# Kernel optimization log

Measured on AMD Instinct MI355X. Metric: run time of the kernel, lower is better.

The kernel has to match this reference:

```python
import jax, jax.numpy as jnp
import numpy as np

B_, N, C = 1024, 64, 512
H = 16          # num_heads
NW = 64         # number of windows (B_ % NW == 0)


def setup_inputs() -> dict:
    key = jax.random.key(0)
    ks = jax.random.split(key, 7)
    return {
        "x": jax.random.normal(ks[0], (B_, N, C), jnp.float32),
        "mask": jax.random.normal(ks[1], (NW, N, N), jnp.float32),
        "qkv_w": jax.random.normal(ks[2], (C, 3 * C), jnp.float32) * 0.02,
        "qkv_b": jax.random.normal(ks[3], (3 * C,), jnp.float32) * 0.02,
        "proj_w": jax.random.normal(ks[4], (C, C), jnp.float32) * 0.02,
        "proj_b": jax.random.normal(ks[5], (C,), jnp.float32) * 0.02,
        "bias_table": jax.random.normal(ks[6], (2 * N - 1, H), jnp.float32) * 0.02,
    }


def reference(x, mask, qkv_w, qkv_b, proj_w, proj_b, bias_table):
    b_, n, c = x.shape
    h = bias_table.shape[1]
    ws = (bias_table.shape[0] + 1) // 2  # window_size, == n here
    d = c // h
    scale = d ** -0.5

    qkv = x @ qkv_w + qkv_b                                   # [B_, N, 3C]
    qkv = qkv.reshape(b_, n, 3, h, d).transpose(2, 0, 3, 1, 4)  # [3, B_, H, N, d]
    q, k, v = qkv[0] * scale, qkv[1], qkv[2]

    attn = jnp.einsum('bhnd,bhmd->bhnm', q, k)                # [B_, H, N, N]

    coords = jnp.arange(ws)
    rel_idx = coords[:, None] - coords[None, :] + ws - 1       # [ws, ws]
    bias = bias_table[rel_idx].transpose(2, 0, 1)              # [H, ws, ws]
    attn = attn + bias[None]

    nw = mask.shape[0]
    attn = attn.reshape(b_ // nw, nw, h, n, n) + mask[None, :, None]
    attn = attn.reshape(-1, h, n, n)
    attn = jax.nn.softmax(attn, axis=-1)

    out = jnp.einsum('bhnm,bhmd->bhnd', attn, v)               # [B_, H, N, d]
    # Faithful to the TF code: v keeps a leading singleton dim after tf.split,
    # so attn@v is [1, B_, H, N, d]; perm [0,2,1,3,4] swaps B_ and H before
    # the final reshape to (B_, N, C).
    out = out[None].transpose(0, 2, 1, 3, 4).reshape(b_, n, c)
    return out @ proj_w + proj_b
```

## Files before the change

kernel.cpp:

```cpp
#include <hip/hip_runtime.h>
#include <hip/hip_bf16.h>
#include <stdint.h>

typedef __attribute__((ext_vector_type(4))) float f32x4;
typedef __attribute__((ext_vector_type(8))) short s16x8;

__device__ __forceinline__ short f2bf(float f) {
  union { float f; uint32_t u; } v; v.f = f;
  uint32_t r = v.u + 0x7FFFu + ((v.u >> 16) & 1u);
  return (short)(r >> 16);
}
__device__ __forceinline__ uint32_t pack2bf(float a, float b) {
  return (uint32_t)(uint16_t)f2bf(a) | ((uint32_t)(uint16_t)f2bf(b) << 16);
}

__device__ __forceinline__ void async16(const void* g, void* l) {
  __builtin_amdgcn_global_load_lds(
      (const __attribute__((address_space(1))) void*)g,
      (__attribute__((address_space(3))) void*)l, 16, 0, 0);
}

__device__ __forceinline__ void transpose_tile(const float* __restrict__ in,
                                               short* __restrict__ out,
                                               int K, int N, int bx, int by, int t) {
  __shared__ float tile[64][65];
  const int tx = t & 63, ty = t >> 6;
#pragma unroll
  for (int r = ty; r < 64; r += 4)
    tile[r][tx] = in[(size_t)(by * 64 + r) * N + bx * 64 + tx];
  __syncthreads();
#pragma unroll
  for (int r = ty; r < 64; r += 4)
    out[(size_t)(bx * 64 + r) * K + by * 64 + tx] = f2bf(tile[tx][r]);
}

__global__ __launch_bounds__(256) void k_prep(const float* __restrict__ x,
                                              short* __restrict__ xbf,
                                              const float* __restrict__ qkv_w,
                                              short* __restrict__ wT,
                                              const float* __restrict__ proj_w,
                                              short* __restrict__ projT) {
  const int bid = blockIdx.x, t = threadIdx.x;
  if (bid < 16384) {
    int i = bid * 256 + t;
    const float4* p = (const float4*)x + (size_t)i * 2;
    float4 a = p[0], b = p[1];
    s16x8 o;
    o[0] = f2bf(a.x); o[1] = f2bf(a.y); o[2] = f2bf(a.z); o[3] = f2bf(a.w);
    o[4] = f2bf(b.x); o[5] = f2bf(b.y); o[6] = f2bf(b.z); o[7] = f2bf(b.w);
    ((s16x8*)xbf)[i] = o;
  } else if (bid < 16384 + 192) {
    int idx = bid - 16384;
    transpose_tile(qkv_w, wT, 512, 1536, idx % 24, idx / 24, t);
  } else {
    int idx = bid - 16384 - 192;
    transpose_tile(proj_w, projT, 512, 512, idx % 8, idx / 8, t);
  }
}

#define TILE_SH 16384

template <int OUTMODE, int NBN, int KK>
__global__ __launch_bounds__(512, 2) void k_gemm256p(const short* __restrict__ A,
                                                     const short* __restrict__ Bw,
                                                     const float* __restrict__ bias,
                                                     void* __restrict__ C,
                                                     int N, int nrounds) {
  __shared__ short lds[2 * 2 * TILE_SH];
  const int t = threadIdx.x;
  const int w = t >> 6, l = t & 63;
  const int wm = w >> 2, wn = w & 3;
  const int swz = (((int)blockIdx.x & 7) << 5) + ((int)blockIdx.x >> 3);

  const int NT = KK >> 6;
  const int NS = nrounds * NT;

  auto stage = [&](const short* __restrict__ G, int row0, int kt, short* dst) {
#pragma unroll
    for (int L = 0; L < 2; ++L) {
      int cw = L * 512 + (t & ~63);
      int c = cw + l;
      int r = c >> 3, s = c & 7;
      async16(G + (size_t)(row0 + r) * KK + kt + ((s ^ (r & 7)) << 3), dst + cw * 8);
    }
  };
  auto issueA = [&](int step, int bmv, int hf) {
    int kt = step & 7;
    stage(A, bmv * 256 + hf * 128, kt * 64, lds + (kt & 1) * 32768 + hf * 8192);
  };
  auto issueB = [&](int step, int bnv, int hf) {
    int kt = step & 7;
    stage(Bw, bnv * 256 + hf * 128, kt * 64, lds + (kt & 1) * 32768 + TILE_SH + hf * 8192);
  };

  const int g = l >> 4, v = l & 7;
  int ofsA[2], ofsB[2];
#pragma unroll
  for (int ks = 0; ks < 2; ++ks) {
    ofsA[ks] = (wm * 128 + (l & 15)) * 64 + (((ks * 4 + g) ^ v) << 3);
    ofsB[ks] = (wn * 64 + (l & 15)) * 64 + (((ks * 4 + g) ^ v) << 3);
  }

  f32x4 acc[8][4] = {};
  s16x8 af[4], bfr[4];

#define RDA4(BASE, KS, AI0)                                           \
  af[0] = *(const s16x8*)((BASE) + ofsA[KS] + ((AI0) + 0) * 1024);    \
  af[1] = *(const s16x8*)((BASE) + ofsA[KS] + ((AI0) + 1) * 1024);    \
  af[2] = *(const s16x8*)((BASE) + ofsA[KS] + ((AI0) + 2) * 1024);    \
  af[3] = *(const s16x8*)((BASE) + ofsA[KS] + ((AI0) + 3) * 1024);

#define RDB4(BASE, KS)                                                \
  bfr[0] = *(const s16x8*)((BASE) + ofsB[KS] + 0 * 1024);             \
  bfr[1] = *(const s16x8*)((BASE) + ofsB[KS] + 1 * 1024);             \
  bfr[2] = *(const s16x8*)((BASE) + ofsB[KS] + 2 * 1024);             \
  bfr[3] = *(const s16x8*)((BASE) + ofsB[KS] + 3 * 1024);

#define MF16(AI0)                                                                                              \
  __builtin_amdgcn_s_setprio(1);                                                                               \
  _Pragma("unroll")                                                                                            \
  for (int nj = 0; nj < 4; ++nj) {                                                                             \
    acc[(AI0) + 0][nj] = __builtin_amdgcn_mfma_f32_16x16x32_bf16(af[0], bfr[nj], acc[(AI0) + 0][nj], 0, 0, 0); \
    acc[(AI0) + 1][nj] = __builtin_amdgcn_mfma_f32_16x16x32_bf16(af[1], bfr[nj], acc[(AI0) + 1][nj], 0, 0, 0); \
    acc[(AI0) + 2][nj] = __builtin_amdgcn_mfma_f32_16x16x32_bf16(af[2], bfr[nj], acc[(AI0) + 2][nj], 0, 0, 0); \
    acc[(AI0) + 3][nj] = __builtin_amdgcn_mfma_f32_16x16x32_bf16(af[3], bfr[nj], acc[(AI0) + 3][nj], 0, 0, 0); \
  }                                                                                                            \
  __builtin_amdgcn_s_setprio(0);

#define PHASE(RD_STMT, STAGE_STMT, AI0, TAIL_STMT)      \
  {                                                     \
    RD_STMT;                                            \
    STAGE_STMT;                                         \
    __builtin_amdgcn_s_barrier();                       \
    asm volatile("s_waitcnt lgkmcnt(0)" ::: "memory");  \
    MF16(AI0);                                          \
    TAIL_STMT;                                          \
    __builtin_amdgcn_s_barrier();                       \
  }

  {
    const int bm0 = swz / NBN, bn0 = swz % NBN;
    issueB(0, bn0, 0); issueB(0, bn0, 1);
    issueA(0, bm0, 0); issueA(0, bm0, 1);
    issueB(1, bn0, 0); issueB(1, bn0, 1);
  }
  asm volatile("s_waitcnt vmcnt(4)" ::: "memory");
  __builtin_amdgcn_s_barrier();

  for (int j = 0; j < nrounds; ++j) {
    const int tauc = swz + (j << 8);
    const int bmc = tauc / NBN, bnc = tauc % NBN;
    for (int T = 0; T < NT; ++T) {
      const int s = (j << 3) + T;
      const int s1 = s + 1, s2 = s + 2;
      const int tau1 = swz + ((s1 >> 3) << 8);
      const int tau2 = swz + ((s2 >> 3) << 8);
      const int bm1 = tau1 / NBN;
      const int bn2 = tau2 % NBN;
      const short* Ab = lds + (T & 1) * 32768;
      const short* Bb = Ab + TILE_SH;

      PHASE(RDB4(Bb, 0); RDA4(Ab, 0, 0), if (s1 < NS) issueA(s1, bm1, 0), 0, );
      PHASE(RDA4(Ab, 0, 4), if (s1 < NS) issueA(s1, bm1, 1), 4, );
      PHASE(RDB4(Bb, 1); RDA4(Ab, 1, 0), if (s2 < NS) issueB(s2, bn2, 0), 0, );
      PHASE(RDA4(Ab, 1, 4), if (s2 < NS) issueB(s2, bn2, 1), 4,
            if (s2 < NS) { asm volatile("s_waitcnt vmcnt(4)" ::: "memory"); }
            else if (s1 < NS) { asm volatile("s_waitcnt vmcnt(0)" ::: "memory"); });
    }

#pragma unroll
    for (int ai = 0; ai < 8; ++ai)
#pragma unroll
      for (int nj = 0; nj < 4; ++nj) {
        int col = bnc * 256 + wn * 64 + nj * 16 + (l & 15);
        float bv = bias[col];
#pragma unroll
        for (int r = 0; r < 4; ++r) {
          int row = bmc * 256 + wm * 128 + ai * 16 + (l >> 4) * 4 + r;
          float vv = acc[ai][nj][r] + bv;
          if (OUTMODE == 1) {
            ((float*)C)[(size_t)row * N + col] = vv;
          } else if (OUTMODE == 0) {
            ((short*)C)[(size_t)row * N + col] = f2bf(vv);
          } else {
            int bb = row >> 6, nn = row & 63;
            int sel = col >> 9, hh = (col >> 5) & 15, dd = col & 31;
            ((short*)C)[(((size_t)(bb * 48 + hh * 3 + sel)) << 11) + (nn << 5) + dd] = f2bf(vv);
          }
        }
      }
#pragma unroll
    for (int ai = 0; ai < 8; ++ai)
#pragma unroll
      for (int nj = 0; nj < 4; ++nj)
        acc[ai][nj] = (f32x4){0.f, 0.f, 0.f, 0.f};
  }
#undef PHASE
#undef MF16
#undef RDA4
#undef RDB4
}

__global__ __launch_bounds__(256) void k_attn(const short* __restrict__ qkv2,
                                              const float* __restrict__ mask,
                                              const float* __restrict__ bias_table,
                                              short* __restrict__ Y) {
  __shared__ __align__(16) float mask_lds[64 * 64];
  __shared__ float bias_lds[4][128];
  __shared__ short p_lds[4][64][72];
  __shared__ short v_lds[4][64][40];

  const int t = threadIdx.x, wv = t >> 6, ln = t & 63;
  const int b = blockIdx.x;
  const int h = blockIdx.y * 4 + wv;
  const int hi = ln >> 4, lo = ln & 15;

  const float4* mk = (const float4*)(mask + (size_t)(b & 63) * 4096);
#pragma unroll
  for (int u = 0; u < 4; ++u) {
    int idx = t + 256 * u;
    int row = idx >> 4, c4 = (idx & 15) * 4;
    *(float4*)&mask_lds[row * 64 + (c4 ^ ((row & 7) << 2))] = mk[idx];
  }
  for (int u = ln; u < 127; u += 64) bias_lds[wv][u] = bias_table[u * 16 + h];

  const short* base = qkv2 + ((size_t)(b * 16 + h)) * 3 * 2048;
  const short* vg = base + 4096;
#pragma unroll
  for (int u = 0; u < 4; ++u) {
    int row = u * 16 + (ln >> 2), c8 = (ln & 3) * 8;
    *(s16x8*)&v_lds[wv][row][c8] = *(const s16x8*)(vg + row * 32 + c8);
  }
  __syncthreads();

  s16x8 qf[4], kf[4];
#pragma unroll
  for (int i = 0; i < 4; ++i) {
    qf[i] = *(const s16x8*)(base + (16 * i + lo) * 32 + hi * 8);
    kf[i] = *(const s16x8*)(base + 2048 + (16 * i + lo) * 32 + hi * 8);
  }
  f32x4 s2[4][4] = {};
#pragma unroll
  for (int j = 0; j < 4; ++j)
#pragma unroll
    for (int i = 0; i < 4; ++i)
      s2[j][i] = __builtin_amdgcn_mfma_f32_16x16x32_bf16(kf[j], qf[i], s2[j][i], 0, 0, 0);

  const float scale = 0.17677669529663687f;
#pragma unroll
  for (int i = 0; i < 4; ++i) {
    const int n = 16 * i + lo;
    const int msw = (n & 7) << 2;
    float x[16];
    float vmax = -1e30f;
#pragma unroll
    for (int j = 0; j < 4; ++j) {
      float4 mrow = *(const float4*)&mask_lds[n * 64 + ((16 * j + 4 * hi) ^ msw)];
#pragma unroll
      for (int r = 0; r < 4; ++r) {
        int m = 16 * j + 4 * hi + r;
        float xx = s2[j][i][r] * scale + bias_lds[wv][n - m + 63] + (&mrow.x)[r];
        x[j * 4 + r] = xx;
        vmax = fmaxf(vmax, xx);
      }
    }
    vmax = fmaxf(vmax, __shfl_xor(vmax, 16, 64));
    vmax = fmaxf(vmax, __shfl_xor(vmax, 32, 64));
    float sum = 0.f;
#pragma unroll
    for (int u = 0; u < 16; ++u) {
      x[u] = __expf(x[u] - vmax);
      sum += x[u];
    }
    sum += __shfl_xor(sum, 16, 64);
    sum += __shfl_xor(sum, 32, 64);
    float rsv = 1.0f / sum;
#pragma unroll
    for (int j = 0; j < 4; ++j)
#pragma unroll
      for (int rp = 0; rp < 2; ++rp)
        *(uint32_t*)&p_lds[wv][n][16 * j + 4 * hi + rp * 2] =
            pack2bf(x[j * 4 + rp * 2] * rsv, x[j * 4 + rp * 2 + 1] * rsv);
  }

  f32x4 o2[2][4] = {};
#pragma unroll
  for (int kk = 0; kk < 2; ++kk) {
    s16x8 pa[4];
#pragma unroll
    for (int i2 = 0; i2 < 4; ++i2)
      pa[i2] = *(const s16x8*)&p_lds[wv][16 * i2 + lo][kk * 32 + hi * 8];
#pragma unroll
    for (int j2 = 0; j2 < 2; ++j2) {
      s16x8 vf;
#pragma unroll
      for (int jj = 0; jj < 8; ++jj)
        vf[jj] = v_lds[wv][kk * 32 + hi * 8 + jj][16 * j2 + lo];
#pragma unroll
      for (int i2 = 0; i2 < 4; ++i2)
        o2[j2][i2] = __builtin_amdgcn_mfma_f32_16x16x32_bf16(vf, pa[i2], o2[j2][i2], 0, 0, 0);
    }
  }

  const int rr = h * 64 + (b >> 4);
#pragma unroll
  for (int i2 = 0; i2 < 4; ++i2) {
    int ss = (b & 15) * 4 + i2;
    short* yr = Y + ((size_t)rr * 64 + ss) * 512 + lo * 32 + 4 * hi;
#pragma unroll
    for (int j2 = 0; j2 < 2; ++j2) {
      uint2 pk;
      pk.x = pack2bf(o2[j2][i2][0], o2[j2][i2][1]);
      pk.y = pack2bf(o2[j2][i2][2], o2[j2][i2][3]);
      *(uint2*)(yr + 16 * j2) = pk;
    }
  }
}

extern "C" void kernel_launch(void* const* d_in, const int* in_sizes, int n_in,
                              void* d_out, int out_size, void* d_ws, size_t ws_size,
                              hipStream_t stream) {
  const float* x      = (const float*)d_in[0];
  const float* mask   = (const float*)d_in[1];
  const float* qkv_w  = (const float*)d_in[2];
  const float* qkv_b  = (const float*)d_in[3];
  const float* proj_w = (const float*)d_in[4];
  const float* proj_b = (const float*)d_in[5];
  const float* btab   = (const float*)d_in[6];
  float* out = (float*)d_out;

  char* w = (char*)d_ws;
  short* qkv_ws = (short*)w;
  short* xbf    = (short*)(w + (size_t)65536 * 1536 * 2);
  short* Y      = xbf;
  short* wT     = (short*)(w + (size_t)65536 * 1536 * 2 + (size_t)65536 * 512 * 2);
  short* projT  = wT + 1536 * 512;

  k_prep<<<16384 + 192 + 64, 256, 0, stream>>>(x, xbf, qkv_w, wT, proj_w, projT);
  k_gemm256p<2, 6, 512><<<256, 512, 0, stream>>>(xbf, wT, qkv_b, qkv_ws, 1536, 6);
  k_attn<<<dim3(1024, 4), 256, 0, stream>>>(qkv_ws, mask, btab, Y);
  k_gemm256p<1, 2, 512><<<256, 512, 0, stream>>>(Y, projT, proj_b, out, 512, 2);
}
```

Baseline: 274.0 us.

## Double-buffer GEMM register fragments and drop per-phase LDS wait barriers

Restructures the GEMM inner loop so LDS fragment reads for the next MFMA group are issued ahead into a second register set (afX/afY, bfrX/bfrY) while the current MFMA group runs. It removes the explicit lgkmcnt(0) wait and the second barrier in each phase, leaving one barrier per phase. The aim is to overlap LDS reads with matrix math and cut synchronisation stalls. In exchange it uses more VGPRs and relies on the compiler's implicit waits and on the remaining barriers for ordering, which risks a race between the async global-to-LDS staging and the fragment reads.

```diff
diff --git a/kernel.cpp b/kernel.cpp
--- a/kernel.cpp
+++ b/kernel.cpp
@@ -102,41 +102,30 @@
   }
 
   f32x4 acc[8][4] = {};
-  s16x8 af[4], bfr[4];
-
-#define RDA4(BASE, KS, AI0)                                           \
-  af[0] = *(const s16x8*)((BASE) + ofsA[KS] + ((AI0) + 0) * 1024);    \
-  af[1] = *(const s16x8*)((BASE) + ofsA[KS] + ((AI0) + 1) * 1024);    \
-  af[2] = *(const s16x8*)((BASE) + ofsA[KS] + ((AI0) + 2) * 1024);    \
-  af[3] = *(const s16x8*)((BASE) + ofsA[KS] + ((AI0) + 3) * 1024);
-
-#define RDB4(BASE, KS)                                                \
-  bfr[0] = *(const s16x8*)((BASE) + ofsB[KS] + 0 * 1024);             \
-  bfr[1] = *(const s16x8*)((BASE) + ofsB[KS] + 1 * 1024);             \
-  bfr[2] = *(const s16x8*)((BASE) + ofsB[KS] + 2 * 1024);             \
-  bfr[3] = *(const s16x8*)((BASE) + ofsB[KS] + 3 * 1024);
-
-#define MF16(AI0)                                                                                              \
+  s16x8 afX[4], afY[4], bfrX[4], bfrY[4];
+
+#define RDA4(D, BASE, KS, AI0)                                        \
+  D[0] = *(const s16x8*)((BASE) + ofsA[KS] + ((AI0) + 0) * 1024);     \
+  D[1] = *(const s16x8*)((BASE) + ofsA[KS] + ((AI0) + 1) * 1024);     \
+  D[2] = *(const s16x8*)((BASE) + ofsA[KS] + ((AI0) + 2) * 1024);     \
+  D[3] = *(const s16x8*)((BASE) + ofsA[KS] + ((AI0) + 3) * 1024);
+
+#define RDB4(D, BASE, KS)                                             \
+  D[0] = *(const s16x8*)((BASE) + ofsB[KS] + 0 * 1024);               \
+  D[1] = *(const s16x8*)((BASE) + ofsB[KS] + 1 * 1024);               \
+  D[2] = *(const s16x8*)((BASE) + ofsB[KS] + 2 * 1024);               \
+  D[3] = *(const s16x8*)((BASE) + ofsB[KS] + 3 * 1024);
+
+#define MF16(AF, BF, AI0)                                                                                      \
   __builtin_amdgcn_s_setprio(1);                                                                               \
   _Pragma("unroll")                                                                                            \
   for (int nj = 0; nj < 4; ++nj) {                                                                             \
-    acc[(AI0) + 0][nj] = __builtin_amdgcn_mfma_f32_16x16x32_bf16(af[0], bfr[nj], acc[(AI0) + 0][nj], 0, 0, 0); \
-    acc[(AI0) + 1][nj] = __builtin_amdgcn_mfma_f32_16x16x32_bf16(af[1], bfr[nj], acc[(AI0) + 1][nj], 0, 0, 0); \
-    acc[(AI0) + 2][nj] = __builtin_amdgcn_mfma_f32_16x16x32_bf16(af[2], bfr[nj], acc[(AI0) + 2][nj], 0, 0, 0); \
-    acc[(AI0) + 3][nj] = __builtin_amdgcn_mfma_f32_16x16x32_bf16(af[3], bfr[nj], acc[(AI0) + 3][nj], 0, 0, 0); \
+    acc[(AI0) + 0][nj] = __builtin_amdgcn_mfma_f32_16x16x32_bf16(AF[0], BF[nj], acc[(AI0) + 0][nj], 0, 0, 0);  \
+    acc[(AI0) + 1][nj] = __builtin_amdgcn_mfma_f32_16x16x32_bf16(AF[1], BF[nj], acc[(AI0) + 1][nj], 0, 0, 0);  \
+    acc[(AI0) + 2][nj] = __builtin_amdgcn_mfma_f32_16x16x32_bf16(AF[2], BF[nj], acc[(AI0) + 2][nj], 0, 0, 0);  \
+    acc[(AI0) + 3][nj] = __builtin_amdgcn_mfma_f32_16x16x32_bf16(AF[3], BF[nj], acc[(AI0) + 3][nj], 0, 0, 0);  \
   }                                                                                                            \
   __builtin_amdgcn_s_setprio(0);
-
-#define PHASE(RD_STMT, STAGE_STMT, AI0, TAIL_STMT)      \
-  {                                                     \
-    RD_STMT;                                            \
-    STAGE_STMT;                                         \
-    __builtin_amdgcn_s_barrier();                       \
-    asm volatile("s_waitcnt lgkmcnt(0)" ::: "memory");  \
-    MF16(AI0);                                          \
-    TAIL_STMT;                                          \
-    __builtin_amdgcn_s_barrier();                       \
-  }
 
   {
     const int bm0 = swz / NBN, bn0 = swz % NBN;
@@ -145,7 +134,6 @@
     issueB(1, bn0, 0); issueB(1, bn0, 1);
   }
   asm volatile("s_waitcnt vmcnt(4)" ::: "memory");
-  __builtin_amdgcn_s_barrier();
 
   for (int j = 0; j < nrounds; ++j) {
     const int tauc = swz + (j << 8);
@@ -160,12 +148,29 @@
       const short* Ab = lds + (T & 1) * 32768;
       const short* Bb = Ab + TILE_SH;
 
-      PHASE(RDB4(Bb, 0); RDA4(Ab, 0, 0), if (s1 < NS) issueA(s1, bm1, 0), 0, );
-      PHASE(RDA4(Ab, 0, 4), if (s1 < NS) issueA(s1, bm1, 1), 4, );
-      PHASE(RDB4(Bb, 1); RDA4(Ab, 1, 0), if (s2 < NS) issueB(s2, bn2, 0), 0, );
-      PHASE(RDA4(Ab, 1, 4), if (s2 < NS) issueB(s2, bn2, 1), 4,
-            if (s2 < NS) { asm volatile("s_waitcnt vmcnt(4)" ::: "memory"); }
-            else if (s1 < NS) { asm volatile("s_waitcnt vmcnt(0)" ::: "memory"); });
+      __builtin_amdgcn_s_barrier();
+      RDB4(bfrX, Bb, 0);
+      RDA4(afX, Ab, 0, 0);
+      RDA4(afY, Ab, 0, 4);
+      if (s1 < NS) issueA(s1, bm1, 0);
+      MF16(afX, bfrX, 0);
+
+      __builtin_amdgcn_s_barrier();
+      RDB4(bfrY, Bb, 1);
+      RDA4(afX, Ab, 1, 0);
+      if (s1 < NS) issueA(s1, bm1, 1);
+      MF16(afY, bfrX, 4);
+
+      __builtin_amdgcn_s_barrier();
+      RDA4(afY, Ab, 1, 4);
+      if (s2 < NS) issueB(s2, bn2, 0);
+      MF16(afX, bfrY, 0);
+
+      __builtin_amdgcn_s_barrier();
+      if (s2 < NS) issueB(s2, bn2, 1);
+      MF16(afY, bfrY, 4);
+      if (s2 < NS) { asm volatile("s_waitcnt vmcnt(4)" ::: "memory"); }
+      else if (s1 < NS) { asm volatile("s_waitcnt vmcnt(0)" ::: "memory"); }
     }
 
 #pragma unroll
@@ -195,7 +200,6 @@
       for (int nj = 0; nj < 4; ++nj)
         acc[ai][nj] = (f32x4){0.f, 0.f, 0.f, 0.f};
   }
-#undef PHASE
 #undef MF16
 #undef RDA4
 #undef RDB4
```

Measured after the change: 300.7 us. 9.8% more time.
